# Performance work log

Hardware: AMD Instinct MI355X
Metric: run time of the kernel (lower is better)

Reference implementation:

```python
import jax, jax.numpy as jnp
import numpy as np

B, GRID, CIN, COUT, TDIM, NMODES = 32, 128, 32, 32, 256, 32
M = NMODES // 2 + 1  # kept modes per axis = 17
FFT_NORM = 'forward'


def setup_inputs() -> dict:
    key = jax.random.key(0)
    ks = jax.random.split(key, 10)
    w_std = float(np.sqrt(1.0 / (2.0 * CIN)))          # normal_initializer(in_co_dim)
    k_std = float(np.sqrt(1.0 / TDIM))                 # ~lecun_normal for Dense kernels
    wshape = (M, M, CIN, COUT)
    return {
        'x': jax.random.normal(ks[0], (B, GRID, GRID, CIN), jnp.float32),
        't_emb': jax.random.normal(ks[1], (B, TDIM), jnp.float32),
        'w1_real': w_std * jax.random.normal(ks[2], wshape, jnp.float32),
        'w1_imag': w_std * jax.random.normal(ks[3], wshape, jnp.float32),
        'w2_real': w_std * jax.random.normal(ks[4], wshape, jnp.float32),
        'w2_imag': w_std * jax.random.normal(ks[5], wshape, jnp.float32),
        'k1_real': k_std * jax.random.normal(ks[6], (TDIM, M), jnp.float32),
        'k1_imag': k_std * jax.random.normal(ks[7], (TDIM, M), jnp.float32),
        'k2_real': k_std * jax.random.normal(ks[8], (TDIM, M), jnp.float32),
        'k2_imag': k_std * jax.random.normal(ks[9], (TDIM, M), jnp.float32),
    }


def reference(x, t_emb, w1_real, w1_imag, w2_real, w2_imag,
              k1_real, k1_imag, k2_real, k2_imag):
    b, n = x.shape[0], x.shape[1]
    # rFFT2 over spatial axes: (b, n, n//2+1, cin) complex
    x_ft = jnp.fft.rfft2(x, axes=(1, 2), norm=FFT_NORM)

    w1 = w1_real + 1j * w1_imag  # (M, M, cin, cout)
    w2 = w2_real + 1j * w2_imag
    # Time modulation: Dense(no bias) -> complex per-mode scale t[b, i].
    # The original builds diag(t) and einsums it into the weights; that equals a
    # simple broadcast scale over the first mode axis, fused here.
    t1 = (t_emb @ k1_real) + 1j * (t_emb @ k1_imag)  # (b, M)
    t2 = (t_emb @ k2_real) + 1j * (t_emb @ k2_imag)

    # Mode-truncated complex channel contraction, scaled by t along axis i.
    xf1 = jnp.einsum('bijc,ijco->bijo', x_ft[:, :M, :M, :], w1) * t1[:, :, None, None]
    xf2 = jnp.einsum('bijc,ijco->bijo', x_ft[:, -M:, :M, :], w2) * t2[:, :, None, None]

    out_ft = jnp.zeros((b, n, n // 2 + 1, COUT), dtype=jnp.complex64)
    out_ft = out_ft.at[:, :M, :M, :].set(xf1)
    out_ft = out_ft.at[:, -M:, :M, :].set(xf2)

    return jnp.fft.irfft2(out_ft, s=(n, n), axes=(1, 2), norm=FFT_NORM)
```

## Files before the change

### kernel.cpp

```cpp
#include <hip/hip_runtime.h>
#include <stdint.h>


#define TWO_PI_OVER_128 0.04908738521234052f

__global__ __launch_bounds__(128) void k_tproj(
    const float* __restrict__ temb, const float* __restrict__ k1r, const float* __restrict__ k1i,
    const float* __restrict__ k2r, const float* __restrict__ k2i, float* __restrict__ tbuf)
{
    int b = blockIdx.x, tid = threadIdx.x;
    __shared__ float ts[256];
    for (int d = tid; d < 256; d += 128) ts[d] = temb[b * 256 + d];
    __syncthreads();
    if (tid < 68) {
        int which = (tid >= 34) ? 1 : 0;
        int rem = tid - which * 34;
        int i = rem >> 1, part = rem & 1;
        const float* kp = which ? (part ? k2i : k2r) : (part ? k1i : k1r);
        float acc = 0.f;
        for (int d = 0; d < 256; ++d) acc += ts[d] * kp[d * 17 + i];
        tbuf[((which * 32 + b) * 17 + i) * 2 + part] = acc;
    }
}

__global__ __launch_bounds__(64) void k_fwd_y(const float* __restrict__ x, float2* __restrict__ T1)
{
    int blk = blockIdx.x;
    int b = blk >> 7, xr = blk & 127;
    __shared__ float xs[128 * 32];
    int tid = threadIdx.x;
    const float4* xv = (const float4*)(x + ((size_t)blk << 12));
    float4* xs4 = (float4*)xs;
#pragma unroll
    for (int i = 0; i < 16; ++i) xs4[tid + (i << 6)] = xv[tid + (i << 6)];
    __syncthreads();
    for (int i = tid; i < 2016; i += 64) {
        int y = (i >> 5) + 1, c = i & 31;
        float a = xs[(y << 5) + c], q = xs[((128 - y) << 5) + c];
        xs[(y << 5) + c] = a + q;
        xs[((128 - y) << 5) + c] = a - q;
    }
    __syncthreads();
    int jg = tid >> 3, cg = tid & 7, c0 = cg << 2;
    float re[2][4] = {{0,0,0,0},{0,0,0,0}}, im[2][4] = {{0,0,0,0},{0,0,0,0}};
    float stc[2], sts[2], cr[2], ci[2];
#pragma unroll
    for (int t = 0; t < 2; ++t) {
        int j = jg + t * 8;
        float sn, cs; sincosf(TWO_PI_OVER_128 * (float)j, &sn, &cs);
        stc[t] = cs; sts[t] = -sn; cr[t] = cs; ci[t] = -sn;
    }
    for (int y = 1; y <= 63; ++y) {
        float4 s = *(const float4*)&xs[(y << 5) + c0];
        float4 d = *(const float4*)&xs[((128 - y) << 5) + c0];
#pragma unroll
        for (int t = 0; t < 2; ++t) {
            re[t][0] = fmaf(s.x, cr[t], re[t][0]);
            re[t][1] = fmaf(s.y, cr[t], re[t][1]);
            re[t][2] = fmaf(s.z, cr[t], re[t][2]);
            re[t][3] = fmaf(s.w, cr[t], re[t][3]);
            im[t][0] = fmaf(d.x, ci[t], im[t][0]);
            im[t][1] = fmaf(d.y, ci[t], im[t][1]);
            im[t][2] = fmaf(d.z, ci[t], im[t][2]);
            im[t][3] = fmaf(d.w, ci[t], im[t][3]);
            float nr = cr[t] * stc[t] - ci[t] * sts[t];
            ci[t] = fmaf(cr[t], sts[t], ci[t] * stc[t]);
            cr[t] = nr;
        }
    }
    const float s_ = 1.f / 16384.f;
    float x0[4], x64[4];
    *(float4*)x0  = *(const float4*)&xs[c0];
    *(float4*)x64 = *(const float4*)&xs[(64 << 5) + c0];
#pragma unroll
    for (int t = 0; t < 2; ++t) {
        int j = jg + t * 8;
        float sg = (j & 1) ? -1.f : 1.f;
        float2* p = T1 + (((size_t)(b * 17 + j) * 128 + xr) << 5) + c0;
        float4 v0 = make_float4((re[t][0] + x0[0] + sg * x64[0]) * s_, im[t][0] * s_,
                                (re[t][1] + x0[1] + sg * x64[1]) * s_, im[t][1] * s_);
        float4 v1 = make_float4((re[t][2] + x0[2] + sg * x64[2]) * s_, im[t][2] * s_,
                                (re[t][3] + x0[3] + sg * x64[3]) * s_, im[t][3] * s_);
        ((float4*)p)[0] = v0; ((float4*)p)[1] = v1;
    }
    if (jg == 0) {
        float re2[4] = {0,0,0,0}, im2[4] = {0,0,0,0};
        const float cs = 0.7071067811865476f, sn = -0.7071067811865476f;
        float cr2 = cs, ci2 = sn;
        for (int y = 1; y <= 63; ++y) {
            float4 s = *(const float4*)&xs[(y << 5) + c0];
            float4 d = *(const float4*)&xs[((128 - y) << 5) + c0];
            re2[0] = fmaf(s.x, cr2, re2[0]); re2[1] = fmaf(s.y, cr2, re2[1]);
            re2[2] = fmaf(s.z, cr2, re2[2]); re2[3] = fmaf(s.w, cr2, re2[3]);
            im2[0] = fmaf(d.x, ci2, im2[0]); im2[1] = fmaf(d.y, ci2, im2[1]);
            im2[2] = fmaf(d.z, ci2, im2[2]); im2[3] = fmaf(d.w, ci2, im2[3]);
            float nr = cr2 * cs - ci2 * sn;
            ci2 = fmaf(cr2, sn, ci2 * cs);
            cr2 = nr;
        }
        float2* p = T1 + (((size_t)(b * 17 + 16) * 128 + xr) << 5) + c0;
        float4 v0 = make_float4((re2[0] + x0[0] + x64[0]) * s_, im2[0] * s_,
                                (re2[1] + x0[1] + x64[1]) * s_, im2[1] * s_);
        float4 v1 = make_float4((re2[2] + x0[2] + x64[2]) * s_, im2[2] * s_,
                                (re2[3] + x0[3] + x64[3]) * s_, im2[3] * s_);
        ((float4*)p)[0] = v0; ((float4*)p)[1] = v1;
    }
}

__global__ __launch_bounds__(512) void k_mid_fused(
    const float2* __restrict__ T1, const float* __restrict__ w1r, const float* __restrict__ w1i,
    const float* __restrict__ w2r, const float* __restrict__ w2i,
    const float* __restrict__ tbuf, float2* __restrict__ U)
{
    int blk = blockIdx.x;
    int b = blk / 17, j = blk - b * 17;
    __shared__ float4 Ts4[2048];
    __shared__ float2 Xf[34 * 32];
    __shared__ float ct[128], st[128];
    int tid = threadIdx.x;
    const float4* s4 = (const float4*)(T1 + (size_t)blk * 4096);
    for (int i = tid; i < 2048; i += 512) Ts4[i] = s4[i];
    if (tid < 128) {
        float a = TWO_PI_OVER_128 * (float)tid;
        sincosf(a, &st[tid], &ct[tid]);
    }
    __syncthreads();
    for (int i = tid; i < 1008; i += 512) {
        int x = (i >> 4) + 1, cp = i & 15;
        float4 a = Ts4[(x << 4) + cp], q = Ts4[((128 - x) << 4) + cp];
        Ts4[(x << 4) + cp] = make_float4(a.x + q.x, a.y + q.y, a.z + q.z, a.w + q.w);
        Ts4[((128 - x) << 4) + cp] = make_float4(a.x - q.x, a.y - q.y, a.z - q.z, a.w - q.w);
    }
    __syncthreads();
    {
        int cp = tid & 15, g = tid >> 4;
        if (g < 16) {
            int f = g + 1;
            float sn, cs; sincosf(TWO_PI_OVER_128 * (float)f, &sn, &cs);
            float cr = cs, ci = sn;
            float P0=0,Q0=0,R0=0,T0=0,P1=0,Q1=0,R1=0,T1a=0;
            for (int x = 1; x <= 63; ++x) {
                float4 S = Ts4[(x << 4) + cp];
                float4 D = Ts4[((128 - x) << 4) + cp];
                P0 = fmaf(S.x, cr, P0); Q0 = fmaf(D.y, ci, Q0);
                R0 = fmaf(S.y, cr, R0); T0 = fmaf(D.x, ci, T0);
                P1 = fmaf(S.z, cr, P1); Q1 = fmaf(D.w, ci, Q1);
                R1 = fmaf(S.w, cr, R1); T1a = fmaf(D.z, ci, T1a);
                float nr = cr * cs - ci * sn;
                ci = fmaf(cr, sn, ci * cs);
                cr = nr;
            }
            float4 t0 = Ts4[cp], t64 = Ts4[(64 << 4) + cp];
            float sg = (f & 1) ? -1.f : 1.f;
            float b0r = t0.x + sg * t64.x, b0i = t0.y + sg * t64.y;
            float b1r = t0.z + sg * t64.z, b1i = t0.w + sg * t64.w;
            int ia = f, ib = 34 - f;
            Xf[ia * 32 + cp*2]   = make_float2(P0 + Q0 + b0r, R0 - T0 + b0i);
            Xf[ia * 32 + cp*2+1] = make_float2(P1 + Q1 + b1r, R1 - T1a + b1i);
            Xf[ib * 32 + cp*2]   = make_float2(P0 - Q0 + b0r, R0 + T0 + b0i);
            Xf[ib * 32 + cp*2+1] = make_float2(P1 - Q1 + b1r, R1 + T1a + b1i);
            if (g == 0) {
                float A0=0,B0=0,A1=0,B1=0;
                for (int x = 1; x <= 63; ++x) {
                    float4 S = Ts4[(x << 4) + cp];
                    A0 += S.x; B0 += S.y; A1 += S.z; B1 += S.w;
                }
                Xf[cp*2]   = make_float2(A0 + t0.x + t64.x, B0 + t0.y + t64.y);
                Xf[cp*2+1] = make_float2(A1 + t0.z + t64.z, B1 + t0.w + t64.w);
            }
            if (g == 8) {
                float sn2, cs2; sincosf(TWO_PI_OVER_128 * 111.f, &sn2, &cs2);
                float cr2 = cs2, ci2 = sn2;
                float p0=0,q0=0,r0=0,s0=0,p1=0,q1=0,r1=0,s1=0;
                for (int x = 1; x <= 63; ++x) {
                    float4 S = Ts4[(x << 4) + cp];
                    float4 D = Ts4[((128 - x) << 4) + cp];
                    p0 = fmaf(S.x, cr2, p0); q0 = fmaf(D.y, ci2, q0);
                    r0 = fmaf(S.y, cr2, r0); s0 = fmaf(D.x, ci2, s0);
                    p1 = fmaf(S.z, cr2, p1); q1 = fmaf(D.w, ci2, q1);
                    r1 = fmaf(S.w, cr2, r1); s1 = fmaf(D.z, ci2, s1);
                    float nr = cr2 * cs2 - ci2 * sn2;
                    ci2 = fmaf(cr2, sn2, ci2 * cs2);
                    cr2 = nr;
                }
                float c0r = t0.x - t64.x, c0i = t0.y - t64.y;
                float c1r = t0.z - t64.z, c1i = t0.w - t64.w;
                Xf[17*32 + cp*2]   = make_float2(p0 + q0 + c0r, r0 - s0 + c0i);
                Xf[17*32 + cp*2+1] = make_float2(p1 + q1 + c1r, r1 - s1 + c1i);
            }
        }
    }
    __syncthreads();
    float2* Ys = (float2*)Ts4;
    {
        int o = tid & 31, gi = tid >> 5;
#pragma unroll
        for (int t = 0; t < 3; ++t) {
            int ii = gi + (t << 4);
            if (ii < 34) {
                int irow = (ii < 17) ? ii : ii - 17;
                const float* wr = ((ii < 17) ? w1r : w2r) + ((irow * 17 + j) << 10) + o;
                const float* wi = ((ii < 17) ? w1i : w2i) + ((irow * 17 + j) << 10) + o;
                float ar = 0.f, ai = 0.f;
#pragma unroll 8
                for (int c = 0; c < 32; ++c) {
                    float2 xv = Xf[ii * 32 + c];
                    float wre = wr[c << 5], wim = wi[c << 5];
                    ar += xv.x * wre - xv.y * wim;
                    ai += xv.x * wim + xv.y * wre;
                }
                int which = (ii >= 17) ? 1 : 0;
                const float* tp = tbuf + ((which * 32 + b) * 17 + irow) * 2;
                float tr = tp[0], ti = tp[1];
                Ys[ii * 32 + o] = make_float2(ar * tr - ai * ti, ar * ti + ai * tr);
            }
        }
    }
    __syncthreads();
    {
        int o = tid & 31, g = tid >> 5;
        float yr[34], yi[34];
#pragma unroll
        for (int i = 0; i < 34; ++i) { float2 v = Ys[i * 32 + o]; yr[i] = v.x; yi[i] = v.y; }
        float2* Ub = U + ((size_t)b * 128 * 17 + j) * 32 + o;
        if (g == 0) {
            float sr = 0.f, si = 0.f;
#pragma unroll
            for (int i = 0; i < 34; ++i) { sr += yr[i]; si += yi[i]; }
            Ub[0] = make_float2(sr, si);
        }
        for (int k = 0; k < 4; ++k) {
            int x = 1 + g + (k << 4);
            if (x == 64) {
                float sr = 0.f, si = 0.f;
#pragma unroll
                for (int i = 0; i < 34; ++i) {
                    float sg2 = (i & 1) ? -1.f : 1.f;
                    sr = fmaf(sg2, yr[i], sr); si = fmaf(sg2, yi[i], si);
                }
                Ub[(size_t)64 * 544] = make_float2(sr, si);
            } else {
                float cx = ct[x], sx = st[x];
                float A1=0,A2=0,A3=0,A4=0;
                float cr = 1.f, ci = 0.f;
#pragma unroll
                for (int i = 0; i < 17; ++i) {
                    A1 = fmaf(yr[i], cr, A1); A4 = fmaf(yr[i], ci, A4);
                    A3 = fmaf(yi[i], cr, A3); A2 = fmaf(yi[i], ci, A2);
                    float nr = cr * cx - ci * sx;
                    ci = fmaf(cr, sx, ci * cx);
                    cr = nr;
                }
                int k2 = (111 * x) & 127;
                cr = ct[k2]; ci = st[k2];
#pragma unroll
                for (int i = 17; i < 34; ++i) {
                    A1 = fmaf(yr[i], cr, A1); A4 = fmaf(yr[i], ci, A4);
                    A3 = fmaf(yi[i], cr, A3); A2 = fmaf(yi[i], ci, A2);
                    float nr = cr * cx - ci * sx;
                    ci = fmaf(cr, sx, ci * cx);
                    cr = nr;
                }
                Ub[(size_t)x * 544]         = make_float2(A1 - A2, A3 + A4);
                Ub[(size_t)(128 - x) * 544] = make_float2(A1 + A2, A3 - A4);
            }
        }
    }
}

__global__ __launch_bounds__(256) void k_fwd_x_mix(
    const float2* __restrict__ T1, const float* __restrict__ w1r, const float* __restrict__ w1i,
    const float* __restrict__ w2r, const float* __restrict__ w2i,
    const float* __restrict__ tbuf, float2* __restrict__ Y)
{
    int blk = blockIdx.x;
    int b = blk / 17, j = blk - b * 17;
    __shared__ float4 Ts4[2048];
    __shared__ float2 Xf[34 * 32];
    int tid = threadIdx.x;
    const float4* s4 = (const float4*)(T1 + (size_t)blk * 4096);
    for (int i = tid; i < 2048; i += 256) Ts4[i] = s4[i];
    __syncthreads();
    {
        int cp = tid & 15, g = tid >> 4;
        int il[3] = {g, g + 16, g + 32};
        float stc[3], sts[3];
#pragma unroll
        for (int t = 0; t < 3; ++t) {
            int i = il[t];
            int f = (i < 17) ? i : i + 94;
            float a = -TWO_PI_OVER_128 * (float)(f & 127);
            sincosf(a, &sts[t], &stc[t]);
        }
        float cr[3] = {1.f, 1.f, 1.f}, ci[3] = {0.f, 0.f, 0.f};
        float r0[3] = {0,0,0}, i0[3] = {0,0,0}, r1[3] = {0,0,0}, i1[3] = {0,0,0};
        const float4* Tc = Ts4 + cp;
#pragma unroll 2
        for (int xx = 0; xx < 128; ++xx) {
            float4 tv = Tc[xx << 4];
#pragma unroll
            for (int t = 0; t < 3; ++t) {
                r0[t] += tv.x * cr[t] - tv.y * ci[t];
                i0[t] += tv.x * ci[t] + tv.y * cr[t];
                r1[t] += tv.z * cr[t] - tv.w * ci[t];
                i1[t] += tv.z * ci[t] + tv.w * cr[t];
                float nr = cr[t] * stc[t] - ci[t] * sts[t];
                ci[t] = fmaf(cr[t], sts[t], ci[t] * stc[t]);
                cr[t] = nr;
            }
        }
#pragma unroll
        for (int t = 0; t < 3; ++t) {
            int i = il[t];
            if (i < 34) {
                Xf[i * 32 + cp * 2]     = make_float2(r0[t], i0[t]);
                Xf[i * 32 + cp * 2 + 1] = make_float2(r1[t], i1[t]);
            }
        }
    }
    __syncthreads();
    {
        int o = tid & 31, gi = tid >> 5;
#pragma unroll
        for (int t = 0; t < 5; ++t) {
            int ii = gi + (t << 3);
            if (ii < 34) {
                int irow = (ii < 17) ? ii : ii - 17;
                const float* wr = ((ii < 17) ? w1r : w2r) + ((irow * 17 + j) << 10) + o;
                const float* wi = ((ii < 17) ? w1i : w2i) + ((irow * 17 + j) << 10) + o;
                float ar = 0.f, ai = 0.f;
#pragma unroll 8
                for (int cc2 = 0; cc2 < 32; ++cc2) {
                    float2 xv = Xf[ii * 32 + cc2];
                    float wre = wr[cc2 << 5];
                    float wim = wi[cc2 << 5];
                    ar += xv.x * wre - xv.y * wim;
                    ai += xv.x * wim + xv.y * wre;
                }
                int which = (ii >= 17) ? 1 : 0;
                const float* tp = tbuf + ((which * 32 + b) * 17 + irow) * 2;
                float tr = tp[0], ti = tp[1];
                Y[(size_t)blk * (34 * 32) + ii * 32 + o] =
                    make_float2(ar * tr - ai * ti, ar * ti + ai * tr);
            }
        }
    }
}

__global__ __launch_bounds__(256) void k_inv_x(const float2* __restrict__ Y, float2* __restrict__ U)
{
    int blk = blockIdx.x;
    int b = blk / 17, j = blk - b * 17;
    __shared__ float2 Ys[34 * 32];
    __shared__ float ct[128], st[128];
    int tid = threadIdx.x;
    if (tid < 128) {
        float a = TWO_PI_OVER_128 * (float)tid;
        sincosf(a, &st[tid], &ct[tid]);
    }
    const float2* src = Y + (size_t)blk * (34 * 32);
    for (int i = tid; i < 34 * 32; i += 256) Ys[i] = src[i];
    __syncthreads();
    int o = tid & 31, g = tid >> 5;
    float yr[34], yi[34];
#pragma unroll
    for (int i = 0; i < 34; ++i) { float2 v = Ys[i * 32 + o]; yr[i] = v.x; yi[i] = v.y; }
    for (int xi = 0; xi < 16; ++xi) {
        int xr = (xi << 3) + g;
        float cx = ct[xr], sx = st[xr];
        float cr = 1.f, ci = 0.f, re = 0.f, im = 0.f;
#pragma unroll
        for (int i = 0; i < 17; ++i) {
            re += yr[i] * cr - yi[i] * ci;
            im += yr[i] * ci + yi[i] * cr;
            float nr = cr * cx - ci * sx;
            ci = fmaf(cr, sx, ci * cx);
            cr = nr;
        }
        int k2 = (111 * xr) & 127;
        cr = ct[k2]; ci = st[k2];
#pragma unroll
        for (int i = 17; i < 34; ++i) {
            re += yr[i] * cr - yi[i] * ci;
            im += yr[i] * ci + yi[i] * cr;
            float nr = cr * cx - ci * sx;
            ci = fmaf(cr, sx, ci * cx);
            cr = nr;
        }
        U[(((size_t)(b * 128 + xr)) * 17 + j) * 32 + o] = make_float2(re, im);
    }
}

__global__ __launch_bounds__(128) void k_inv_y(const float2* __restrict__ U, float* __restrict__ out)
{
    int blk = blockIdx.x;
    __shared__ float2 Us[17 * 32];
    int tid = threadIdx.x;
    const float4* src4 = (const float4*)(U + (size_t)blk * 544);
    float4* Us4 = (float4*)Us;
    for (int i = tid; i < 272; i += 128) Us4[i] = src4[i];
    __syncthreads();
    int cg = tid & 15, yg = tid >> 4, c0 = cg << 1;
    float base0, base1;
    {
        float4 v = *(const float4*)&Us[c0];
        base0 = v.x; base1 = v.z;
    }
    float urr[16][2], uii[16][2];
#pragma unroll
    for (int j = 1; j <= 16; ++j) {
        float4 v = *(const float4*)&Us[j * 32 + c0];
        urr[j-1][0] = 2.f * v.x; uii[j-1][0] = 2.f * v.y;
        urr[j-1][1] = 2.f * v.z; uii[j-1][1] = 2.f * v.w;
    }
    float* op = out + ((size_t)blk << 12);
    for (int k = 0; k < 9; ++k) {
        int y = yg + (k << 3);
        if (y > 64) break;
        float cy, sy; sincosf(TWO_PI_OVER_128 * (float)y, &sy, &cy);
        float cr = cy, ci = sy;
        float A0 = 0.f, A1 = 0.f, B0 = 0.f, B1 = 0.f;
#pragma unroll
        for (int j = 0; j < 16; ++j) {
            A0 = fmaf(urr[j][0], cr, A0);
            B0 = fmaf(uii[j][0], ci, B0);
            A1 = fmaf(urr[j][1], cr, A1);
            B1 = fmaf(uii[j][1], ci, B1);
            float nr = cr * cy - ci * sy;
            ci = fmaf(cr, sy, ci * cy);
            cr = nr;
        }
        *(float2*)&op[(y << 5) + c0] = make_float2(base0 + A0 - B0, base1 + A1 - B1);
        if (y > 0 && y < 64)
            *(float2*)&op[((128 - y) << 5) + c0] = make_float2(base0 + A0 + B0, base1 + A1 + B1);
    }
}

extern "C" void kernel_launch(void* const* d_in, const int* in_sizes, int n_in,
                              void* d_out, int out_size, void* d_ws, size_t ws_size,
                              hipStream_t stream)
{
    const float* x    = (const float*)d_in[0];
    const float* temb = (const float*)d_in[1];
    const float* w1r  = (const float*)d_in[2];
    const float* w1i  = (const float*)d_in[3];
    const float* w2r  = (const float*)d_in[4];
    const float* w2i  = (const float*)d_in[5];
    const float* k1r  = (const float*)d_in[6];
    const float* k1i  = (const float*)d_in[7];
    const float* k2r  = (const float*)d_in[8];
    const float* k2i  = (const float*)d_in[9];
    float* out = (float*)d_out;

    char* ws = (char*)d_ws;
    const size_t T1_BYTES = 17825792;
    const size_t NEED_FUSED = 2 * T1_BYTES + 8704;

    if (ws_size >= NEED_FUSED) {
        float2* T1 = (float2*)ws;
        float2* U  = (float2*)(ws + T1_BYTES);
        float*  tb = (float*)(ws + 2 * T1_BYTES);
        k_tproj    <<<32,   128, 0, stream>>>(temb, k1r, k1i, k2r, k2i, tb);
        k_fwd_y    <<<4096, 64,  0, stream>>>(x, T1);
        k_mid_fused<<<544,  512, 0, stream>>>(T1, w1r, w1i, w2r, w2i, tb, U);
        k_inv_y    <<<4096, 128, 0, stream>>>(U, out);
    } else {
        float2* T1 = (float2*)ws;
        float2* Yb = (float2*)(ws + T1_BYTES);
        float*  tb = (float*)(ws + T1_BYTES + 4734976);
        float2* U  = T1;
        k_tproj    <<<32,   128, 0, stream>>>(temb, k1r, k1i, k2r, k2i, tb);
        k_fwd_y    <<<4096, 64,  0, stream>>>(x, T1);
        k_fwd_x_mix<<<544,  256, 0, stream>>>(T1, w1r, w1i, w2r, w2i, tb, Yb);
        k_inv_x    <<<544,  256, 0, stream>>>(Yb, U);
        k_inv_y    <<<4096, 128, 0, stream>>>(U, out);
    }
}
```

Measured before the change: 213.0 us.

## Replace twiddle recurrences with shared-memory sincos tables and rebalance mid-kernel work

Replaces the per-iteration complex-multiply twiddle recurrences in the forward-y, mid and inverse-y DFT loops with lookups into a 128-entry shared cos/sin table, indexed by modular integer accumulation. In the fused mid kernel, the DC and Nyquist-row DFTs move to their own thread groups instead of serial extra work on existing threads. The channel-mixing GEMM now has each thread compute four outputs using float4 weight loads. The tproj reduction is split across four accumulators. The goal is fewer ALU ops and dependent chains and better load balance, at the cost of extra LDS reads and table setup.

```diff
diff --git a/kernel.cpp b/kernel.cpp
--- a/kernel.cpp
+++ b/kernel.cpp
@@ -17,9 +17,14 @@
         int rem = tid - which * 34;
         int i = rem >> 1, part = rem & 1;
         const float* kp = which ? (part ? k2i : k2r) : (part ? k1i : k1r);
-        float acc = 0.f;
-        for (int d = 0; d < 256; ++d) acc += ts[d] * kp[d * 17 + i];
-        tbuf[((which * 32 + b) * 17 + i) * 2 + part] = acc;
+        float a0 = 0.f, a1 = 0.f, a2 = 0.f, a3 = 0.f;
+        for (int d = 0; d < 256; d += 4) {
+            a0 = fmaf(ts[d],     kp[(d)     * 17 + i], a0);
+            a1 = fmaf(ts[d + 1], kp[(d + 1) * 17 + i], a1);
+            a2 = fmaf(ts[d + 2], kp[(d + 2) * 17 + i], a2);
+            a3 = fmaf(ts[d + 3], kp[(d + 3) * 17 + i], a3);
+        }
+        tbuf[((which * 32 + b) * 17 + i) * 2 + part] = (a0 + a1) + (a2 + a3);
     }
 }
 
@@ -28,7 +33,14 @@
     int blk = blockIdx.x;
     int b = blk >> 7, xr = blk & 127;
     __shared__ float xs[128 * 32];
+    __shared__ float2 cst[128];
     int tid = threadIdx.x;
+    {
+        float s0, c0; sincosf(TWO_PI_OVER_128 * (float)tid, &s0, &c0);
+        cst[tid] = make_float2(c0, -s0);
+        float s1, c1; sincosf(TWO_PI_OVER_128 * (float)(tid + 64), &s1, &c1);
+        cst[tid + 64] = make_float2(c1, -s1);
+    }
     const float4* xv = (const float4*)(x + ((size_t)blk << 12));
     float4* xs4 = (float4*)xs;
 #pragma unroll
@@ -43,30 +55,30 @@
     __syncthreads();
     int jg = tid >> 3, cg = tid & 7, c0 = cg << 2;
     float re[2][4] = {{0,0,0,0},{0,0,0,0}}, im[2][4] = {{0,0,0,0},{0,0,0,0}};
-    float stc[2], sts[2], cr[2], ci[2];
-#pragma unroll
-    for (int t = 0; t < 2; ++t) {
-        int j = jg + t * 8;
-        float sn, cs; sincosf(TWO_PI_OVER_128 * (float)j, &sn, &cs);
-        stc[t] = cs; sts[t] = -sn; cr[t] = cs; ci[t] = -sn;
-    }
+    int j0 = jg, j1 = jg + 8;
+    int idx0 = 0, idx1 = 0;
     for (int y = 1; y <= 63; ++y) {
+        idx0 = (idx0 + j0) & 127;
+        idx1 = (idx1 + j1) & 127;
+        float2 w0 = cst[idx0], w1 = cst[idx1];
         float4 s = *(const float4*)&xs[(y << 5) + c0];
         float4 d = *(const float4*)&xs[((128 - y) << 5) + c0];
-#pragma unroll
-        for (int t = 0; t < 2; ++t) {
-            re[t][0] = fmaf(s.x, cr[t], re[t][0]);
-            re[t][1] = fmaf(s.y, cr[t], re[t][1]);
-            re[t][2] = fmaf(s.z, cr[t], re[t][2]);
-            re[t][3] = fmaf(s.w, cr[t], re[t][3]);
-            im[t][0] = fmaf(d.x, ci[t], im[t][0]);
-            im[t][1] = fmaf(d.y, ci[t], im[t][1]);
-            im[t][2] = fmaf(d.z, ci[t], im[t][2]);
-            im[t][3] = fmaf(d.w, ci[t], im[t][3]);
-            float nr = cr[t] * stc[t] - ci[t] * sts[t];
-            ci[t] = fmaf(cr[t], sts[t], ci[t] * stc[t]);
-            cr[t] = nr;
-        }
+        re[0][0] = fmaf(s.x, w0.x, re[0][0]);
+        re[0][1] = fmaf(s.y, w0.x, re[0][1]);
+        re[0][2] = fmaf(s.z, w0.x, re[0][2]);
+        re[0][3] = fmaf(s.w, w0.x, re[0][3]);
+        im[0][0] = fmaf(d.x, w0.y, im[0][0]);
+        im[0][1] = fmaf(d.y, w0.y, im[0][1]);
+        im[0][2] = fmaf(d.z, w0.y, im[0][2]);
+        im[0][3] = fmaf(d.w, w0.y, im[0][3]);
+        re[1][0] = fmaf(s.x, w1.x, re[1][0]);
+        re[1][1] = fmaf(s.y, w1.x, re[1][1]);
+        re[1][2] = fmaf(s.z, w1.x, re[1][2]);
+        re[1][3] = fmaf(s.w, w1.x, re[1][3]);
+        im[1][0] = fmaf(d.x, w1.y, im[1][0]);
+        im[1][1] = fmaf(d.y, w1.y, im[1][1]);
+        im[1][2] = fmaf(d.z, w1.y, im[1][2]);
+        im[1][3] = fmaf(d.w, w1.y, im[1][3]);
     }
     const float s_ = 1.f / 16384.f;
     float x0[4], x64[4];
@@ -85,18 +97,16 @@
     }
     if (jg == 0) {
         float re2[4] = {0,0,0,0}, im2[4] = {0,0,0,0};
-        const float cs = 0.7071067811865476f, sn = -0.7071067811865476f;
-        float cr2 = cs, ci2 = sn;
+        int idx2 = 0;
         for (int y = 1; y <= 63; ++y) {
+            idx2 = (idx2 + 16) & 127;
+            float2 w = cst[idx2];
             float4 s = *(const float4*)&xs[(y << 5) + c0];
             float4 d = *(const float4*)&xs[((128 - y) << 5) + c0];
-            re2[0] = fmaf(s.x, cr2, re2[0]); re2[1] = fmaf(s.y, cr2, re2[1]);
-            re2[2] = fmaf(s.z, cr2, re2[2]); re2[3] = fmaf(s.w, cr2, re2[3]);
-            im2[0] = fmaf(d.x, ci2, im2[0]); im2[1] = fmaf(d.y, ci2, im2[1]);
-            im2[2] = fmaf(d.z, ci2, im2[2]); im2[3] = fmaf(d.w, ci2, im2[3]);
-            float nr = cr2 * cs - ci2 * sn;
-            ci2 = fmaf(cr2, sn, ci2 * cs);
-            cr2 = nr;
+            re2[0] = fmaf(s.x, w.x, re2[0]); re2[1] = fmaf(s.y, w.x, re2[1]);
+            re2[2] = fmaf(s.z, w.x, re2[2]); re2[3] = fmaf(s.w, w.x, re2[3]);
+            im2[0] = fmaf(d.x, w.y, im2[0]); im2[1] = fmaf(d.y, w.y, im2[1]);
+            im2[2] = fmaf(d.z, w.y, im2[2]); im2[3] = fmaf(d.w, w.y, im2[3]);
         }
         float2* p = T1 + (((size_t)(b * 17 + 16) * 128 + xr) << 5) + c0;
         float4 v0 = make_float4((re2[0] + x0[0] + x64[0]) * s_, im2[0] * s_,
@@ -116,41 +126,39 @@
     int b = blk / 17, j = blk - b * 17;
     __shared__ float4 Ts4[2048];
     __shared__ float2 Xf[34 * 32];
-    __shared__ float ct[128], st[128];
+    __shared__ float2 cst[128];
     int tid = threadIdx.x;
     const float4* s4 = (const float4*)(T1 + (size_t)blk * 4096);
     for (int i = tid; i < 2048; i += 512) Ts4[i] = s4[i];
     if (tid < 128) {
-        float a = TWO_PI_OVER_128 * (float)tid;
-        sincosf(a, &st[tid], &ct[tid]);
+        float s, c; sincosf(TWO_PI_OVER_128 * (float)tid, &s, &c);
+        cst[tid] = make_float2(c, s);
     }
     __syncthreads();
     for (int i = tid; i < 1008; i += 512) {
-        int x = (i >> 4) + 1, cp = i & 15;
-        float4 a = Ts4[(x << 4) + cp], q = Ts4[((128 - x) << 4) + cp];
-        Ts4[(x << 4) + cp] = make_float4(a.x + q.x, a.y + q.y, a.z + q.z, a.w + q.w);
-        Ts4[((128 - x) << 4) + cp] = make_float4(a.x - q.x, a.y - q.y, a.z - q.z, a.w - q.w);
-    }
-    __syncthreads();
-    {
-        int cp = tid & 15, g = tid >> 4;
-        if (g < 16) {
-            int f = g + 1;
-            float sn, cs; sincosf(TWO_PI_OVER_128 * (float)f, &sn, &cs);
-            float cr = cs, ci = sn;
+        int xx = (i >> 4) + 1, cp = i & 15;
+        float4 a = Ts4[(xx << 4) + cp], q = Ts4[((128 - xx) << 4) + cp];
+        Ts4[(xx << 4) + cp] = make_float4(a.x + q.x, a.y + q.y, a.z + q.z, a.w + q.w);
+        Ts4[((128 - xx) << 4) + cp] = make_float4(a.x - q.x, a.y - q.y, a.z - q.z, a.w - q.w);
+    }
+    __syncthreads();
+    if (tid < 288) {
+        int cp = tid & 15, u = tid >> 4;
+        float4 t0 = Ts4[cp], t64 = Ts4[(64 << 4) + cp];
+        if (u < 16) {
+            int f = u + 1;
+            int idx = 0;
             float P0=0,Q0=0,R0=0,T0=0,P1=0,Q1=0,R1=0,T1a=0;
-            for (int x = 1; x <= 63; ++x) {
-                float4 S = Ts4[(x << 4) + cp];
-                float4 D = Ts4[((128 - x) << 4) + cp];
-                P0 = fmaf(S.x, cr, P0); Q0 = fmaf(D.y, ci, Q0);
-                R0 = fmaf(S.y, cr, R0); T0 = fmaf(D.x, ci, T0);
-                P1 = fmaf(S.z, cr, P1); Q1 = fmaf(D.w, ci, Q1);
-                R1 = fmaf(S.w, cr, R1); T1a = fmaf(D.z, ci, T1a);
-                float nr = cr * cs - ci * sn;
-                ci = fmaf(cr, sn, ci * cs);
-                cr = nr;
-            }
-            float4 t0 = Ts4[cp], t64 = Ts4[(64 << 4) + cp];
+            for (int xx = 1; xx <= 63; ++xx) {
+                idx = (idx + f) & 127;
+                float2 w = cst[idx];
+                float4 S = Ts4[(xx << 4) + cp];
+                float4 D = Ts4[((128 - xx) << 4) + cp];
+                P0 = fmaf(S.x, w.x, P0); Q0 = fmaf(D.y, w.y, Q0);
+                R0 = fmaf(S.y, w.x, R0); T0 = fmaf(D.x, w.y, T0);
+                P1 = fmaf(S.z, w.x, P1); Q1 = fmaf(D.w, w.y, Q1);
+                R1 = fmaf(S.w, w.x, R1); T1a = fmaf(D.z, w.y, T1a);
+            }
             float sg = (f & 1) ? -1.f : 1.f;
             float b0r = t0.x + sg * t64.x, b0i = t0.y + sg * t64.y;
             float b1r = t0.z + sg * t64.z, b1i = t0.w + sg * t64.w;
@@ -159,62 +167,66 @@
             Xf[ia * 32 + cp*2+1] = make_float2(P1 + Q1 + b1r, R1 - T1a + b1i);
             Xf[ib * 32 + cp*2]   = make_float2(P0 - Q0 + b0r, R0 + T0 + b0i);
             Xf[ib * 32 + cp*2+1] = make_float2(P1 - Q1 + b1r, R1 + T1a + b1i);
-            if (g == 0) {
-                float A0=0,B0=0,A1=0,B1=0;
-                for (int x = 1; x <= 63; ++x) {
-                    float4 S = Ts4[(x << 4) + cp];
-                    A0 += S.x; B0 += S.y; A1 += S.z; B1 += S.w;
-                }
-                Xf[cp*2]   = make_float2(A0 + t0.x + t64.x, B0 + t0.y + t64.y);
-                Xf[cp*2+1] = make_float2(A1 + t0.z + t64.z, B1 + t0.w + t64.w);
-            }
-            if (g == 8) {
-                float sn2, cs2; sincosf(TWO_PI_OVER_128 * 111.f, &sn2, &cs2);
-                float cr2 = cs2, ci2 = sn2;
-                float p0=0,q0=0,r0=0,s0=0,p1=0,q1=0,r1=0,s1=0;
-                for (int x = 1; x <= 63; ++x) {
-                    float4 S = Ts4[(x << 4) + cp];
-                    float4 D = Ts4[((128 - x) << 4) + cp];
-                    p0 = fmaf(S.x, cr2, p0); q0 = fmaf(D.y, ci2, q0);
-                    r0 = fmaf(S.y, cr2, r0); s0 = fmaf(D.x, ci2, s0);
-                    p1 = fmaf(S.z, cr2, p1); q1 = fmaf(D.w, ci2, q1);
-                    r1 = fmaf(S.w, cr2, r1); s1 = fmaf(D.z, ci2, s1);
-                    float nr = cr2 * cs2 - ci2 * sn2;
-                    ci2 = fmaf(cr2, sn2, ci2 * cs2);
-                    cr2 = nr;
-                }
-                float c0r = t0.x - t64.x, c0i = t0.y - t64.y;
-                float c1r = t0.z - t64.z, c1i = t0.w - t64.w;
-                Xf[17*32 + cp*2]   = make_float2(p0 + q0 + c0r, r0 - s0 + c0i);
-                Xf[17*32 + cp*2+1] = make_float2(p1 + q1 + c1r, r1 - s1 + c1i);
-            }
+        } else if (u == 16) {
+            float A0=0,B0=0,A1=0,B1=0;
+            for (int xx = 1; xx <= 63; ++xx) {
+                float4 S = Ts4[(xx << 4) + cp];
+                A0 += S.x; B0 += S.y; A1 += S.z; B1 += S.w;
+            }
+            Xf[cp*2]   = make_float2(A0 + t0.x + t64.x, B0 + t0.y + t64.y);
+            Xf[cp*2+1] = make_float2(A1 + t0.z + t64.z, B1 + t0.w + t64.w);
+        } else {
+            int idx = 0;
+            float p0=0,q0=0,r0=0,s0=0,p1=0,q1=0,r1=0,s1=0;
+            for (int xx = 1; xx <= 63; ++xx) {
+                idx = (idx + 111) & 127;
+                float2 w = cst[idx];
+                float4 S = Ts4[(xx << 4) + cp];
+                float4 D = Ts4[((128 - xx) << 4) + cp];
+                p0 = fmaf(S.x, w.x, p0); q0 = fmaf(D.y, w.y, q0);
+                r0 = fmaf(S.y, w.x, r0); s0 = fmaf(D.x, w.y, s0);
+                p1 = fmaf(S.z, w.x, p1); q1 = fmaf(D.w, w.y, q1);
+                r1 = fmaf(S.w, w.x, r1); s1 = fmaf(D.z, w.y, s1);
+            }
+            float c0r = t0.x - t64.x, c0i = t0.y - t64.y;
+            float c1r = t0.z - t64.z, c1i = t0.w - t64.w;
+            Xf[17*32 + cp*2]   = make_float2(p0 + q0 + c0r, r0 - s0 + c0i);
+            Xf[17*32 + cp*2+1] = make_float2(p1 + q1 + c1r, r1 - s1 + c1i);
         }
     }
     __syncthreads();
     float2* Ys = (float2*)Ts4;
-    {
-        int o = tid & 31, gi = tid >> 5;
-#pragma unroll
-        for (int t = 0; t < 3; ++t) {
-            int ii = gi + (t << 4);
-            if (ii < 34) {
-                int irow = (ii < 17) ? ii : ii - 17;
-                const float* wr = ((ii < 17) ? w1r : w2r) + ((irow * 17 + j) << 10) + o;
-                const float* wi = ((ii < 17) ? w1i : w2i) + ((irow * 17 + j) << 10) + o;
-                float ar = 0.f, ai = 0.f;
-#pragma unroll 8
-                for (int c = 0; c < 32; ++c) {
-                    float2 xv = Xf[ii * 32 + c];
-                    float wre = wr[c << 5], wim = wi[c << 5];
-                    ar += xv.x * wre - xv.y * wim;
-                    ai += xv.x * wim + xv.y * wre;
-                }
-                int which = (ii >= 17) ? 1 : 0;
-                const float* tp = tbuf + ((which * 32 + b) * 17 + irow) * 2;
-                float tr = tp[0], ti = tp[1];
-                Ys[ii * 32 + o] = make_float2(ar * tr - ai * ti, ar * ti + ai * tr);
-            }
-        }
+    if (tid < 272) {
+        int oq = tid & 7, ii = tid >> 3;
+        int o0 = oq << 2;
+        int irow = (ii < 17) ? ii : ii - 17;
+        const float* wr = ((ii < 17) ? w1r : w2r) + ((irow * 17 + j) << 10) + o0;
+        const float* wi = ((ii < 17) ? w1i : w2i) + ((irow * 17 + j) << 10) + o0;
+        float ar0=0,ai0=0,ar1=0,ai1=0,ar2=0,ai2=0,ar3=0,ai3=0;
+#pragma unroll 4
+        for (int c = 0; c < 32; ++c) {
+            float2 xv = Xf[ii * 32 + c];
+            float4 wre = *(const float4*)(wr + (c << 5));
+            float4 wim = *(const float4*)(wi + (c << 5));
+            ar0 = fmaf(xv.x, wre.x, ar0); ar0 = fmaf(-xv.y, wim.x, ar0);
+            ai0 = fmaf(xv.x, wim.x, ai0); ai0 = fmaf( xv.y, wre.x, ai0);
+            ar1 = fmaf(xv.x, wre.y, ar1); ar1 = fmaf(-xv.y, wim.y, ar1);
+            ai1 = fmaf(xv.x, wim.y, ai1); ai1 = fmaf( xv.y, wre.y, ai1);
+            ar2 = fmaf(xv.x, wre.z, ar2); ar2 = fmaf(-xv.y, wim.z, ar2);
+            ai2 = fmaf(xv.x, wim.z, ai2); ai2 = fmaf( xv.y, wre.z, ai2);
+            ar3 = fmaf(xv.x, wre.w, ar3); ar3 = fmaf(-xv.y, wim.w, ar3);
+            ai3 = fmaf(xv.x, wim.w, ai3); ai3 = fmaf( xv.y, wre.w, ai3);
+        }
+        int which = (ii >= 17) ? 1 : 0;
+        const float* tp = tbuf + ((which * 32 + b) * 17 + irow) * 2;
+        float tr = tp[0], ti = tp[1];
+        float2* yp = Ys + ii * 32 + o0;
+        float4 y01 = make_float4(ar0 * tr - ai0 * ti, ar0 * ti + ai0 * tr,
+                                 ar1 * tr - ai1 * ti, ar1 * ti + ai1 * tr);
+        float4 y23 = make_float4(ar2 * tr - ai2 * ti, ar2 * ti + ai2 * tr,
+                                 ar3 * tr - ai3 * ti, ar3 * ti + ai3 * tr);
+        ((float4*)yp)[0] = y01;
+        ((float4*)yp)[1] = y23;
     }
     __syncthreads();
     {
@@ -240,26 +252,22 @@
                 }
                 Ub[(size_t)64 * 544] = make_float2(sr, si);
             } else {
-                float cx = ct[x], sx = st[x];
                 float A1=0,A2=0,A3=0,A4=0;
-                float cr = 1.f, ci = 0.f;
+                int idx = 0;
 #pragma unroll
                 for (int i = 0; i < 17; ++i) {
-                    A1 = fmaf(yr[i], cr, A1); A4 = fmaf(yr[i], ci, A4);
-                    A3 = fmaf(yi[i], cr, A3); A2 = fmaf(yi[i], ci, A2);
-                    float nr = cr * cx - ci * sx;
-                    ci = fmaf(cr, sx, ci * cx);
-                    cr = nr;
+                    float2 w = cst[idx];
+                    A1 = fmaf(yr[i], w.x, A1); A4 = fmaf(yr[i], w.y, A4);
+                    A3 = fmaf(yi[i], w.x, A3); A2 = fmaf(yi[i], w.y, A2);
+                    idx = (idx + x) & 127;
                 }
-                int k2 = (111 * x) & 127;
-                cr = ct[k2]; ci = st[k2];
+                idx = (111 * x) & 127;
 #pragma unroll
                 for (int i = 17; i < 34; ++i) {
-                    A1 = fmaf(yr[i], cr, A1); A4 = fmaf(yr[i], ci, A4);
-                    A3 = fmaf(yi[i], cr, A3); A2 = fmaf(yi[i], ci, A2);
-                    float nr = cr * cx - ci * sx;
-                    ci = fmaf(cr, sx, ci * cx);
-                    cr = nr;
+                    float2 w = cst[idx];
+                    A1 = fmaf(yr[i], w.x, A1); A4 = fmaf(yr[i], w.y, A4);
+                    A3 = fmaf(yi[i], w.x, A3); A2 = fmaf(yi[i], w.y, A2);
+                    idx = (idx + x) & 127;
                 }
                 Ub[(size_t)x * 544]         = make_float2(A1 - A2, A3 + A4);
                 Ub[(size_t)(128 - x) * 544] = make_float2(A1 + A2, A3 - A4);
@@ -395,7 +403,12 @@
 {
     int blk = blockIdx.x;
     __shared__ float2 Us[17 * 32];
+    __shared__ float2 cst[128];
     int tid = threadIdx.x;
+    {
+        float s, c; sincosf(TWO_PI_OVER_128 * (float)tid, &s, &c);
+        cst[tid] = make_float2(c, s);
+    }
     const float4* src4 = (const float4*)(U + (size_t)blk * 544);
     float4* Us4 = (float4*)Us;
     for (int i = tid; i < 272; i += 128) Us4[i] = src4[i];
@@ -408,27 +421,25 @@
     }
     float urr[16][2], uii[16][2];
 #pragma unroll
-    for (int j = 1; j <= 16; ++j) {
-        float4 v = *(const float4*)&Us[j * 32 + c0];
-        urr[j-1][0] = 2.f * v.x; uii[j-1][0] = 2.f * v.y;
-        urr[j-1][1] = 2.f * v.z; uii[j-1][1] = 2.f * v.w;
+    for (int jj = 1; jj <= 16; ++jj) {
+        float4 v = *(const float4*)&Us[jj * 32 + c0];
+        urr[jj-1][0] = 2.f * v.x; uii[jj-1][0] = 2.f * v.y;
+        urr[jj-1][1] = 2.f * v.z; uii[jj-1][1] = 2.f * v.w;
     }
     float* op = out + ((size_t)blk << 12);
     for (int k = 0; k < 9; ++k) {
         int y = yg + (k << 3);
         if (y > 64) break;
-        float cy, sy; sincosf(TWO_PI_OVER_128 * (float)y, &sy, &cy);
-        float cr = cy, ci = sy;
         float A0 = 0.f, A1 = 0.f, B0 = 0.f, B1 = 0.f;
-#pragma unroll
-        for (int j = 0; j < 16; ++j) {
-            A0 = fmaf(urr[j][0], cr, A0);
-            B0 = fmaf(uii[j][0], ci, B0);
-            A1 = fmaf(urr[j][1], cr, A1);
-            B1 = fmaf(uii[j][1], ci, B1);
-            float nr = cr * cy - ci * sy;
-            ci = fmaf(cr, sy, ci * cy);
-            cr = nr;
+        int idx = y;
+#pragma unroll
+        for (int jj = 0; jj < 16; ++jj) {
+            float2 w = cst[idx];
+            A0 = fmaf(urr[jj][0], w.x, A0);
+            B0 = fmaf(uii[jj][0], w.y, B0);
+            A1 = fmaf(urr[jj][1], w.x, A1);
+            B1 = fmaf(uii[jj][1], w.y, B1);
+            idx = (idx + y) & 127;
         }
         *(float2*)&op[(y << 5) + c0] = make_float2(base0 + A0 - B0, base1 + A1 - B1);
         if (y > 0 && y < 64)
```

Result: faster. 198.2 us (-7.0%).
